# Performance work log

Hardware: AMD Instinct MI355X
Metric: run time of the kernel (lower is better)

The kernel has to match this reference:

```python
import jax, jax.numpy as jnp
import numpy as np

N_NODES = 100000
N_EDGES = 1600000
D_IN = 128
D_OUT = 128


def setup_inputs() -> dict:
    key = jax.random.key(0)
    k = jax.random.split(key, 6)
    x = jax.random.normal(k[0], (N_NODES, D_IN), dtype=jnp.float32)
    edge_src = jax.random.randint(k[1], (N_EDGES,), 0, N_NODES, dtype=jnp.int64)
    edge_dst = jax.random.randint(k[2], (N_EDGES,), 0, N_NODES, dtype=jnp.int64)
    edge_weight = jax.random.uniform(k[3], (N_EDGES,), dtype=jnp.float32)
    # xavier-uniform-ish init for the two projection matrices
    lim = float(np.sqrt(6.0 / (D_IN + D_OUT)))
    W_nbrs = jax.random.uniform(k[4], (D_IN, D_OUT), minval=-lim, maxval=lim, dtype=jnp.float32)
    W_self = jax.random.uniform(k[5], (D_IN, D_OUT), minval=-lim, maxval=lim, dtype=jnp.float32)
    bias = jnp.zeros((D_OUT,), dtype=jnp.float32)
    return {"x": x, "edge_src": edge_src, "edge_dst": edge_dst,
            "edge_weight": edge_weight, "W_nbrs": W_nbrs, "W_self": W_self,
            "bias": bias}


def reference(x, edge_src, edge_dst, edge_weight, W_nbrs, W_self, bias):
    # y = x @ W_nbrs  (dense projection)
    y = x @ W_nbrs                                   # [N, D_OUT]
    # spmm(adj, y): out[i] = sum_{(j->i) in E} w_ij * y[j]
    msgs = edge_weight[:, None] * y[edge_src]        # [E, D_OUT]
    agg = jax.ops.segment_sum(msgs, edge_dst, num_segments=x.shape[0])
    # self transform + bias
    return agg + x @ W_self + bias
```

## Files before the change

kernel.cpp:

```cpp
#include <hip/hip_runtime.h>
#include <hip/hip_bf16.h>

#define D 128

typedef __bf16 bf16x8 __attribute__((ext_vector_type(8)));
typedef unsigned short u16x8 __attribute__((ext_vector_type(8)));
typedef float f32x4 __attribute__((ext_vector_type(4)));

__device__ __forceinline__ unsigned short f2bf(float f) {
    unsigned u = __float_as_uint(f);
    u += 0x7FFFu + ((u >> 16) & 1u);
    return (unsigned short)(u >> 16);
}
__device__ __forceinline__ float bf2f(unsigned u16) {
    return __uint_as_float(u16 << 16);
}

__global__ void k_build_wt(const float* __restrict__ Wn, const float* __restrict__ Ws,
                           unsigned short* __restrict__ WTs,
                           int* __restrict__ cnt, int N) {
    int g = blockIdx.x * blockDim.x + threadIdx.x;
    int k = g >> 8;
    int c = g & 255;
    float v = (c < 128) ? Wn[k * 128 + c] : Ws[k * 128 + (c - 128)];
    int chunk = k >> 3;
    WTs[c * 128 + (((chunk ^ (c & 15)) << 3) | (k & 7))] = f2bf(v);
    for (int i = g; i < N; i += 32768) cnt[i] = 0;
}

__global__ __launch_bounds__(256) void k_gemm_rank(
    const float* __restrict__ x, const unsigned short* __restrict__ WTs,
    const float* __restrict__ bias, int N,
    unsigned short* __restrict__ y, float* __restrict__ out,
    const int* __restrict__ edst, int E,
    int* __restrict__ cnt, int* __restrict__ rank) {
    __shared__ unsigned short sm[128 * 128];
    int b = blockIdx.x;
    int tid = threadIdx.x;
    if (b & 1) {
        int e0 = (b >> 1) * 1024 + tid;
        #pragma unroll
        for (int k = 0; k < 4; ++k) {
            int e = e0 + k * 256;
            if (e < E) {
                int d = edst[e];
                rank[e] = atomicAdd(&cnt[d], 1);
            }
        }
        return;
    }
    int gb = b >> 1;
    int brow = gb * 64;
    if (brow >= N) return;
    int w = tid >> 6, l = tid & 63;
    int row0 = brow + w * 16;
    int c15 = l & 15;
    int kgrp = l >> 4;
    const uint4* gs = (const uint4*)WTs;
    uint4* ss = (uint4*)sm;
    {
        #pragma unroll
        for (int r = 0; r < 8; ++r) ss[r * 256 + tid] = gs[r * 256 + tid];
    }
    int arow = row0 + c15;
    bool avalid = (arow < N);
    const float* xr = x + (size_t)arow * D;
    bf16x8 afrag[4];
    #pragma unroll
    for (int ks = 0; ks < 4; ++ks) {
        int k0 = ks * 32 + kgrp * 8;
        float4 a0, a1;
        if (avalid) { a0 = *(const float4*)(xr + k0); a1 = *(const float4*)(xr + k0 + 4); }
        else { a0 = make_float4(0.f, 0.f, 0.f, 0.f); a1 = a0; }
        bf16x8 f;
        f[0] = (__bf16)a0.x; f[1] = (__bf16)a0.y; f[2] = (__bf16)a0.z; f[3] = (__bf16)a0.w;
        f[4] = (__bf16)a1.x; f[5] = (__bf16)a1.y; f[6] = (__bf16)a1.z; f[7] = (__bf16)a1.w;
        afrag[ks] = f;
    }
    __syncthreads();
    int orow = row0 + kgrp * 4;
    f32x4 acc[8];
    #pragma unroll
    for (int nt = 0; nt < 8; ++nt) {
        int c = nt * 16 + c15;
        f32x4 a = {0.f, 0.f, 0.f, 0.f};
        #pragma unroll
        for (int ks = 0; ks < 4; ++ks) {
            int chunk = ks * 4 + kgrp;
            const bf16x8* bp = (const bf16x8*)(sm + c * 128 + ((chunk ^ c15) << 3));
            a = __builtin_amdgcn_mfma_f32_16x16x32_bf16(afrag[ks], *bp, a, 0, 0, 0);
        }
        acc[nt] = a;
    }
    #pragma unroll
    for (int j = 0; j < 4; ++j) {
        int r = orow + j;
        if (r < N) {
            u16x8 f;
            #pragma unroll
            for (int nt = 0; nt < 8; ++nt) f[nt] = f2bf(acc[nt][j]);
            *(u16x8*)(y + (size_t)r * D + c15 * 8) = f;
        }
    }
    __syncthreads();
    {
        #pragma unroll
        for (int r = 0; r < 8; ++r) ss[r * 256 + tid] = gs[2048 + r * 256 + tid];
    }
    __syncthreads();
    #pragma unroll
    for (int nt = 0; nt < 8; ++nt) {
        int c = nt * 16 + c15;
        f32x4 a = {0.f, 0.f, 0.f, 0.f};
        #pragma unroll
        for (int ks = 0; ks < 4; ++ks) {
            int chunk = ks * 4 + kgrp;
            const bf16x8* bp = (const bf16x8*)(sm + c * 128 + ((chunk ^ c15) << 3));
            a = __builtin_amdgcn_mfma_f32_16x16x32_bf16(afrag[ks], *bp, a, 0, 0, 0);
        }
        acc[nt] = a;
    }
    __syncthreads();
    float* smf = (float*)sm;
    int lr0 = w * 16 + kgrp * 4;
    #pragma unroll
    for (int nt = 0; nt < 8; ++nt) {
        #pragma unroll
        for (int j = 0; j < 4; ++j)
            smf[(lr0 + j) * 128 + nt * 16 + c15] = acc[nt][j];
    }
    __syncthreads();
    float4 bv = *(const float4*)&bias[(tid * 4) & 127];
    #pragma unroll
    for (int k = 0; k < 8; ++k) {
        int f = tid * 4 + k * 1024;
        int gr = brow + (f >> 7);
        if (gr < N) {
            float4 c4 = *(float4*)&smf[f];
            c4.x += bv.x; c4.y += bv.y; c4.z += bv.z; c4.w += bv.w;
            *(float4*)(out + (size_t)brow * D + f) = c4;
        }
    }
}

__global__ void k_scanA(const int* __restrict__ cnt, int N,
                        int* __restrict__ ofs, int* __restrict__ bsum) {
    __shared__ int lds[1024];
    int t = threadIdx.x, i = blockIdx.x * 1024 + t;
    int v = (i < N) ? cnt[i] : 0;
    lds[t] = v; __syncthreads();
    for (int d = 1; d < 1024; d <<= 1) {
        int x = (t >= d) ? lds[t - d] : 0; __syncthreads();
        lds[t] += x; __syncthreads();
    }
    if (i < N) ofs[i] = lds[t] - v;
    if (t == 1023) bsum[blockIdx.x] = lds[t];
}

__global__ void k_scanB(int* __restrict__ bsum, int NB) {
    __shared__ int lds[128];
    int t = threadIdx.x;
    int v = (t < NB) ? bsum[t] : 0;
    lds[t] = v; __syncthreads();
    for (int d = 1; d < 128; d <<= 1) {
        int x = (t >= d) ? lds[t - d] : 0; __syncthreads();
        lds[t] += x; __syncthreads();
    }
    if (t < NB) bsum[t] = lds[t] - v;
}

__global__ __launch_bounds__(256) void k_fill(
    const int* __restrict__ src, const int* __restrict__ dst,
    const float* __restrict__ w, const int* __restrict__ rank, int E,
    const int* __restrict__ ofs, const int* __restrict__ bsum,
    uint2* __restrict__ sorted) {
    int e = blockIdx.x * blockDim.x + threadIdx.x;
    if (e < E) {
        int d = dst[e];
        int pos = ofs[d] + bsum[d >> 10] + rank[e];
        sorted[pos] = make_uint2((unsigned)src[e], __float_as_uint(w[e]));
    }
}

__global__ __launch_bounds__(256) void k_agg(
    const unsigned short* __restrict__ y, const uint2* __restrict__ sorted,
    const int* __restrict__ ofs, const int* __restrict__ bsum,
    const int* __restrict__ cnt, int N,
    float* __restrict__ out) {
    int w = threadIdx.x >> 6, l = threadIdx.x & 63;
    int node = blockIdx.x * 4 + w;
    if (node >= N) return;
    int s = ofs[node] + bsum[node >> 10], n = cnt[node];
    int g = l >> 4, li = l & 15;
    const uint2* sp = sorted + s;
    float a0 = 0.f, a1 = 0.f, a2 = 0.f, a3 = 0.f;
    float a4 = 0.f, a5 = 0.f, a6 = 0.f, a7 = 0.f;
    int j = g;
    for (; j + 4 < n; j += 8) {
        uint2 pa = sp[j];
        uint2 pb = sp[j + 4];
        uint4 va = *(const uint4*)(y + (size_t)pa.x * D + li * 8);
        uint4 vb = *(const uint4*)(y + (size_t)pb.x * D + li * 8);
        float wa = __uint_as_float(pa.y), wb = __uint_as_float(pb.y);
        a0 += wa * bf2f(va.x & 0xFFFFu); a1 += wa * bf2f(va.x >> 16);
        a2 += wa * bf2f(va.y & 0xFFFFu); a3 += wa * bf2f(va.y >> 16);
        a4 += wa * bf2f(va.z & 0xFFFFu); a5 += wa * bf2f(va.z >> 16);
        a6 += wa * bf2f(va.w & 0xFFFFu); a7 += wa * bf2f(va.w >> 16);
        a0 += wb * bf2f(vb.x & 0xFFFFu); a1 += wb * bf2f(vb.x >> 16);
        a2 += wb * bf2f(vb.y & 0xFFFFu); a3 += wb * bf2f(vb.y >> 16);
        a4 += wb * bf2f(vb.z & 0xFFFFu); a5 += wb * bf2f(vb.z >> 16);
        a6 += wb * bf2f(vb.w & 0xFFFFu); a7 += wb * bf2f(vb.w >> 16);
    }
    if (j < n) {
        uint2 p = sp[j];
        uint4 v = *(const uint4*)(y + (size_t)p.x * D + li * 8);
        float wt = __uint_as_float(p.y);
        a0 += wt * bf2f(v.x & 0xFFFFu); a1 += wt * bf2f(v.x >> 16);
        a2 += wt * bf2f(v.y & 0xFFFFu); a3 += wt * bf2f(v.y >> 16);
        a4 += wt * bf2f(v.z & 0xFFFFu); a5 += wt * bf2f(v.z >> 16);
        a6 += wt * bf2f(v.w & 0xFFFFu); a7 += wt * bf2f(v.w >> 16);
    }
    a0 += __shfl_xor(a0, 16, 64); a1 += __shfl_xor(a1, 16, 64);
    a2 += __shfl_xor(a2, 16, 64); a3 += __shfl_xor(a3, 16, 64);
    a4 += __shfl_xor(a4, 16, 64); a5 += __shfl_xor(a5, 16, 64);
    a6 += __shfl_xor(a6, 16, 64); a7 += __shfl_xor(a7, 16, 64);
    a0 += __shfl_xor(a0, 32, 64); a1 += __shfl_xor(a1, 32, 64);
    a2 += __shfl_xor(a2, 32, 64); a3 += __shfl_xor(a3, 32, 64);
    a4 += __shfl_xor(a4, 32, 64); a5 += __shfl_xor(a5, 32, 64);
    a6 += __shfl_xor(a6, 32, 64); a7 += __shfl_xor(a7, 32, 64);
    if (l < 16) {
        float* op = out + (size_t)node * D + li;
        op[0]   += a0; op[16]  += a1; op[32]  += a2; op[48]  += a3;
        op[64]  += a4; op[80]  += a5; op[96]  += a6; op[112] += a7;
    }
}

extern "C" void kernel_launch(void* const* d_in, const int* in_sizes, int n_in,
                              void* d_out, int out_size, void* d_ws, size_t ws_size,
                              hipStream_t stream) {
    const float* x    = (const float*)d_in[0];
    const int*   esrc = (const int*)d_in[1];
    const int*   edst = (const int*)d_in[2];
    const float* ew   = (const float*)d_in[3];
    const float* Wn   = (const float*)d_in[4];
    const float* Wsf  = (const float*)d_in[5];
    const float* bias = (const float*)d_in[6];
    float* out = (float*)d_out;
    int N = in_sizes[0] / D;
    int E = in_sizes[1];

    char* ws = (char*)d_ws;
    size_t off = 0;
    unsigned short* WTs = (unsigned short*)(ws + off); off += 256 * 128 * sizeof(unsigned short);
    unsigned short* yb  = (unsigned short*)(ws + off); off += (size_t)N * D * sizeof(unsigned short);
    off = (off + 255) & ~(size_t)255;
    int* cnt  = (int*)(ws + off); off += (size_t)N * 4; off = (off + 255) & ~(size_t)255;
    int* ofs  = (int*)(ws + off); off += (size_t)N * 4; off = (off + 255) & ~(size_t)255;
    int* bsum = (int*)(ws + off); off += 1024;
    int* rank = (int*)(ws + off); off += (size_t)E * 4; off = (off + 255) & ~(size_t)255;
    uint2* sorted = (uint2*)(ws + off); off += (size_t)E * 8;

    k_build_wt<<<128, 256, 0, stream>>>(Wn, Wsf, WTs, cnt, N);

    int GB = (N + 63) / 64;
    int RB = (E + 1023) / 1024;
    int G2 = (GB > RB ? GB : RB) * 2;
    k_gemm_rank<<<G2, 256, 0, stream>>>(x, WTs, bias, N, yb, out,
                                        edst, E, cnt, rank);

    int NB = (N + 1023) / 1024;
    k_scanA<<<NB, 1024, 0, stream>>>(cnt, N, ofs, bsum);
    k_scanB<<<1, 128, 0, stream>>>(bsum, NB);
    k_fill<<<(E + 255) / 256, 256, 0, stream>>>(esrc, edst, ew, rank, E, ofs, bsum, sorted);

    k_agg<<<(N + 3) / 4, 256, 0, stream>>>(yb, sorted, ofs, bsum, cnt, N, out);
}
```

Baseline: 293.3 us.

## Drop LDS staging in projection GEMM and write outputs straight from registers

```diff
diff --git a/kernel.cpp b/kernel.cpp
--- a/kernel.cpp
+++ b/kernel.cpp
@@ -20,11 +20,10 @@
                            unsigned short* __restrict__ WTs,
                            int* __restrict__ cnt, int N) {
     int g = blockIdx.x * blockDim.x + threadIdx.x;
-    int k = g >> 8;
-    int c = g & 255;
+    int c = g >> 7;
+    int k = g & 127;
     float v = (c < 128) ? Wn[k * 128 + c] : Ws[k * 128 + (c - 128)];
-    int chunk = k >> 3;
-    WTs[c * 128 + (((chunk ^ (c & 15)) << 3) | (k & 7))] = f2bf(v);
+    WTs[c * 128 + k] = f2bf(v);
     for (int i = g; i < N; i += 32768) cnt[i] = 0;
 }
 
@@ -34,7 +33,6 @@
     unsigned short* __restrict__ y, float* __restrict__ out,
     const int* __restrict__ edst, int E,
     int* __restrict__ cnt, int* __restrict__ rank) {
-    __shared__ unsigned short sm[128 * 128];
     int b = blockIdx.x;
     int tid = threadIdx.x;
     if (b & 1) {
@@ -42,10 +40,7 @@
         #pragma unroll
         for (int k = 0; k < 4; ++k) {
             int e = e0 + k * 256;
-            if (e < E) {
-                int d = edst[e];
-                rank[e] = atomicAdd(&cnt[d], 1);
-            }
+            if (e < E) rank[e] = atomicAdd(&cnt[edst[e]], 1);
         }
         return;
     }
@@ -56,12 +51,6 @@
     int row0 = brow + w * 16;
     int c15 = l & 15;
     int kgrp = l >> 4;
-    const uint4* gs = (const uint4*)WTs;
-    uint4* ss = (uint4*)sm;
-    {
-        #pragma unroll
-        for (int r = 0; r < 8; ++r) ss[r * 256 + tid] = gs[r * 256 + tid];
-    }
     int arow = row0 + c15;
     bool avalid = (arow < N);
     const float* xr = x + (size_t)arow * D;
@@ -77,17 +66,15 @@
         f[4] = (__bf16)a1.x; f[5] = (__bf16)a1.y; f[6] = (__bf16)a1.z; f[7] = (__bf16)a1.w;
         afrag[ks] = f;
     }
-    __syncthreads();
     int orow = row0 + kgrp * 4;
+    const unsigned short* Bbase = WTs + (size_t)c15 * 128 + kgrp * 8;
     f32x4 acc[8];
     #pragma unroll
     for (int nt = 0; nt < 8; ++nt) {
-        int c = nt * 16 + c15;
         f32x4 a = {0.f, 0.f, 0.f, 0.f};
         #pragma unroll
         for (int ks = 0; ks < 4; ++ks) {
-            int chunk = ks * 4 + kgrp;
-            const bf16x8* bp = (const bf16x8*)(sm + c * 128 + ((chunk ^ c15) << 3));
+            const bf16x8* bp = (const bf16x8*)(Bbase + nt * 16 * 128 + ks * 32);
             a = __builtin_amdgcn_mfma_f32_16x16x32_bf16(afrag[ks], *bp, a, 0, 0, 0);
         }
         acc[nt] = a;
@@ -102,43 +89,29 @@
             *(u16x8*)(y + (size_t)r * D + c15 * 8) = f;
         }
     }
-    __syncthreads();
-    {
-        #pragma unroll
-        for (int r = 0; r < 8; ++r) ss[r * 256 + tid] = gs[2048 + r * 256 + tid];
-    }
-    __syncthreads();
     #pragma unroll
     for (int nt = 0; nt < 8; ++nt) {
-        int c = nt * 16 + c15;
         f32x4 a = {0.f, 0.f, 0.f, 0.f};
         #pragma unroll
         for (int ks = 0; ks < 4; ++ks) {
-            int chunk = ks * 4 + kgrp;
-            const bf16x8* bp = (const bf16x8*)(sm + c * 128 + ((chunk ^ c15) << 3));
+            const bf16x8* bp = (const bf16x8*)(Bbase + (128 + nt * 16) * 128 + ks * 32);
             a = __builtin_amdgcn_mfma_f32_16x16x32_bf16(afrag[ks], *bp, a, 0, 0, 0);
         }
         acc[nt] = a;
     }
-    __syncthreads();
-    float* smf = (float*)sm;
-    int lr0 = w * 16 + kgrp * 4;
-    #pragma unroll
-    for (int nt = 0; nt < 8; ++nt) {
-        #pragma unroll
-        for (int j = 0; j < 4; ++j)
-            smf[(lr0 + j) * 128 + nt * 16 + c15] = acc[nt][j];
-    }
-    __syncthreads();
-    float4 bv = *(const float4*)&bias[(tid * 4) & 127];
-    #pragma unroll
-    for (int k = 0; k < 8; ++k) {
-        int f = tid * 4 + k * 1024;
-        int gr = brow + (f >> 7);
-        if (gr < N) {
-            float4 c4 = *(float4*)&smf[f];
-            c4.x += bv.x; c4.y += bv.y; c4.z += bv.z; c4.w += bv.w;
-            *(float4*)(out + (size_t)brow * D + f) = c4;
+    float bv[8];
+    #pragma unroll
+    for (int nt = 0; nt < 8; ++nt) bv[nt] = bias[nt * 16 + c15];
+    #pragma unroll
+    for (int j = 0; j < 4; ++j) {
+        int r = orow + j;
+        if (r < N) {
+            float4 s0 = make_float4(acc[0][j] + bv[0], acc[1][j] + bv[1],
+                                    acc[2][j] + bv[2], acc[3][j] + bv[3]);
+            float4 s1 = make_float4(acc[4][j] + bv[4], acc[5][j] + bv[5],
+                                    acc[6][j] + bv[6], acc[7][j] + bv[7]);
+            float4* op = (float4*)(out + (size_t)r * D + c15 * 8);
+            op[0] = s0; op[1] = s1;
         }
     }
 }
@@ -174,11 +147,15 @@
     const float* __restrict__ w, const int* __restrict__ rank, int E,
     const int* __restrict__ ofs, const int* __restrict__ bsum,
     uint2* __restrict__ sorted) {
-    int e = blockIdx.x * blockDim.x + threadIdx.x;
-    if (e < E) {
-        int d = dst[e];
-        int pos = ofs[d] + bsum[d >> 10] + rank[e];
-        sorted[pos] = make_uint2((unsigned)src[e], __float_as_uint(w[e]));
+    int e0 = blockIdx.x * 1024 + threadIdx.x;
+    #pragma unroll
+    for (int k = 0; k < 4; ++k) {
+        int e = e0 + k * 256;
+        if (e < E) {
+            int d = dst[e];
+            int pos = ofs[d] + bsum[d >> 10] + rank[e];
+            sorted[pos] = make_uint2((unsigned)src[e], __float_as_uint(w[e]));
+        }
     }
 }
 
@@ -192,6 +169,11 @@
     if (node >= N) return;
     int s = ofs[node] + bsum[node >> 10], n = cnt[node];
     int g = l >> 4, li = l & 15;
+    float4 s0, s1;
+    if (l < 16) {
+        const float4* spf = (const float4*)(out + (size_t)node * D + li * 8);
+        s0 = spf[0]; s1 = spf[1];
+    }
     const uint2* sp = sorted + s;
     float a0 = 0.f, a1 = 0.f, a2 = 0.f, a3 = 0.f;
     float a4 = 0.f, a5 = 0.f, a6 = 0.f, a7 = 0.f;
@@ -230,8 +212,10 @@
     a6 += __shfl_xor(a6, 32, 64); a7 += __shfl_xor(a7, 32, 64);
     if (l < 16) {
         float* op = out + (size_t)node * D + li;
-        op[0]   += a0; op[16]  += a1; op[32]  += a2; op[48]  += a3;
-        op[64]  += a4; op[80]  += a5; op[96]  += a6; op[112] += a7;
+        op[0]   = a0 + s0.x; op[16]  = a1 + s0.y;
+        op[32]  = a2 + s0.z; op[48]  = a3 + s0.w;
+        op[64]  = a4 + s1.x; op[80]  = a5 + s1.y;
+        op[96]  = a6 + s1.z; op[112] = a7 + s1.w;
     }
 }
 
@@ -271,7 +255,7 @@
     int NB = (N + 1023) / 1024;
     k_scanA<<<NB, 1024, 0, stream>>>(cnt, N, ofs, bsum);
     k_scanB<<<1, 128, 0, stream>>>(bsum, NB);
-    k_fill<<<(E + 255) / 256, 256, 0, stream>>>(esrc, edst, ew, rank, E, ofs, bsum, sorted);
+    k_fill<<<(E + 1023) / 1024, 256, 0, stream>>>(esrc, edst, ew, rank, E, ofs, bsum, sorted);
 
     k_agg<<<(N + 3) / 4, 256, 0, stream>>>(yb, sorted, ofs, bsum, cnt, N, out);
 }
```

New measurement: 352.0 us. 1.2x slower.
